# Optimization experiments

Measured on AMD Instinct MI355X. Metric: run time of the kernel, lower is better.

Reference implementation:

```python
import jax, jax.numpy as jnp
import numpy as np

ALPHA = 5.0  # spatial bandwidth
BETA = 5.0   # feature (bilateral) bandwidth
EPS = 1e-20


def gauss_filter(features, values):
    """Exact dense Gaussian (bilateral) filter: the math the permutohedral
    lattice (pl.apply) approximates.
    features: [B, D, N], values: [B, C, N] -> [B, C, N]
    Q[b,c,i] = sum_j exp(-0.5*||f_i - f_j||^2) * v[b,c,j]
    """
    sq = jnp.sum(features * features, axis=1)  # [B, N]
    d2 = sq[:, :, None] + sq[:, None, :] - 2.0 * jnp.einsum('bdi,bdj->bij', features, features)
    K = jnp.exp(-0.5 * jnp.maximum(d2, 0.0))  # [B, N, N]
    return jnp.einsum('bij,bcj->bci', K, values)


def setup_inputs() -> dict:
    key = jax.random.key(0)
    k1, k2 = jax.random.split(key)
    I = jax.random.normal(k1, (2, 3, 18, 18, 18), dtype=jnp.float32)
    U = jax.random.normal(k2, (2, 4, 18, 18, 18), dtype=jnp.float32)
    return {"I": I, "U": U}


def reference(I, U):
    B, n_feat, X, Y, Z = I.shape
    N = X * Y * Z
    n_ch = U.shape[1]
    # spatial coordinates, scaled by alpha (smoothness kernel part)
    gx, gy, gz = jnp.meshgrid(jnp.arange(X), jnp.arange(Y), jnp.arange(Z), indexing='ij')
    coords = jnp.stack([gx, gy, gz], 0).astype(I.dtype)            # [3, X, Y, Z]
    coords = jnp.broadcast_to(coords[None], (B, 3, X, Y, Z))
    feats = jnp.concatenate([coords / ALPHA, I / BETA], axis=1)    # [B, 3+n_feat, X, Y, Z]
    feats = feats.reshape(B, n_feat + 3, N)
    # normalization: filter an all-ones signal (use_norm=True path)
    ones = jnp.ones((B, 1, N), dtype=I.dtype)
    spatial_norm = 1.0 / jnp.sqrt(gauss_filter(feats, ones) + EPS)  # [B, 1, N]
    # unary -> softmax over channels
    Uf = U.reshape(B, n_ch, N)
    H1 = jax.nn.softmax(Uf, axis=1)                                 # [B, C, N]
    # pairwise message passing (normalized bilateral filter)
    Q1 = gauss_filter(feats, H1 * spatial_norm) * spatial_norm      # [B, C, N]
    # trace(Q1_flat.T @ (1 - H1_flat)) == elementwise sum (same reshape on both)
    loss = jnp.sum(Q1 * (1.0 - H1))
    return loss
```

## Files before the change

kernel.cpp:

```cpp
#include <hip/hip_runtime.h>

#define B_      2
#define NCH     4
#define DIMX    18
#define NPT     (18*18*18)
#define TIL     183
#define ITIL    184
#define NPTP    (ITIL*32)
#define IBLOCKS 23
#define JSP     22
#define NB      (IBLOCKS*JSP*B_)
#define MAXT    9
#define FSC     (1.2011224087864498f / 5.0f)
#define QPAD    -30000.0f

typedef __attribute__((ext_vector_type(8)))  short short8;
typedef __attribute__((ext_vector_type(16))) float f32x16;
typedef __attribute__((ext_vector_type(4)))  int   int4_;

#define EXP2(x) __builtin_amdgcn_exp2f(x)
#define MFMA32(a, b, c) __builtin_amdgcn_mfma_f32_32x32x16_bf16(a, b, c, 0, 0, 0)

__device__ __forceinline__ unsigned short bf16rtn(float f) {
  unsigned u = __float_as_uint(f);
  u += 0x7fffu + ((u >> 16) & 1u);
  return (unsigned short)(u >> 16);
}
__device__ __forceinline__ float bf2f(unsigned short s) {
  return __uint_as_float(((unsigned)s) << 16);
}

__device__ __forceinline__ float blockReduceSum(float v) {
  #pragma unroll
  for (int o = 32; o > 0; o >>= 1) v += __shfl_down(v, o, 64);
  __shared__ float red[4];
  int wid = threadIdx.x >> 6, lane = threadIdx.x & 63;
  if (lane == 0) red[wid] = v;
  __syncthreads();
  v = (threadIdx.x < 4) ? red[threadIdx.x] : 0.0f;
  if (wid == 0) {
    v += __shfl_down(v, 2, 64);
    v += __shfl_down(v, 1, 64);
  }
  __syncthreads();
  return v;
}

__device__ __forceinline__ void feat6(const float* __restrict__ I, int bb, int n,
                                      float f[6], float* q) {
  int x = n / (DIMX * DIMX);
  int rem = n - x * DIMX * DIMX;
  int y = rem / DIMX, zz = rem - y * DIMX;
  f[0] = x * FSC; f[1] = y * FSC; f[2] = zz * FSC;
  f[3] = I[(size_t)(bb * 3 + 0) * NPT + n] * FSC;
  f[4] = I[(size_t)(bb * 3 + 1) * NPT + n] * FSC;
  f[5] = I[(size_t)(bb * 3 + 2) * NPT + n] * FSC;
  *q = -0.5f * (f[0]*f[0] + f[1]*f[1] + f[2]*f[2] + f[3]*f[3] + f[4]*f[4] + f[5]*f[5]);
}

__device__ __forceinline__ void bfeat(const float* __restrict__ I, int bb, int n,
                                      short8* hi, short8* lo) {
  short8 h_ = {0,0,0,0,0,0,0,0}, l_ = {0,0,0,0,0,0,0,0};
  if (n < NPT) {
    float f[6], q;
    feat6(I, bb, n, f, &q);
    float bv[8] = {f[0], f[1], f[2], f[3], f[4], f[5], 1.0f, q};
    #pragma unroll
    for (int e = 0; e < 8; ++e) {
      unsigned short bh = bf16rtn(bv[e]);
      h_[e] = (short)bh;
      l_[e] = (short)bf16rtn(bv[e] - bf2f(bh));
    }
  } else {
    h_[7] = (short)bf16rtn(QPAD);
  }
  *hi = h_; *lo = l_;
}

__device__ __forceinline__ short8 afeat(const float* __restrict__ I, int bb, int n) {
  short8 a = {0,0,0,0,0,0,0,0};
  if (n < NPT) {
    float f[6], q;
    feat6(I, bb, n, f, &q);
    float av[8] = {f[0], f[1], f[2], f[3], f[4], f[5], q, 1.0f};
    #pragma unroll
    for (int e = 0; e < 8; ++e) a[e] = (short)bf16rtn(av[e]);
  }
  return a;
}

__device__ __forceinline__ float4 softmax4(const float* __restrict__ U, int bb, int n) {
  float u0 = U[(size_t)(bb * NCH + 0) * NPT + n];
  float u1 = U[(size_t)(bb * NCH + 1) * NPT + n];
  float u2 = U[(size_t)(bb * NCH + 2) * NPT + n];
  float u3 = U[(size_t)(bb * NCH + 3) * NPT + n];
  float m = fmaxf(fmaxf(u0, u1), fmaxf(u2, u3));
  float e0 = __expf(u0-m), e1 = __expf(u1-m), e2 = __expf(u2-m), e3 = __expf(u3-m);
  float inv = 1.0f / (e0 + e1 + e2 + e3);
  return make_float4(e0*inv, e1*inv, e2*inv, e3*inv);
}

__device__ __forceinline__ float expsum16(const f32x16 acc) {
  float e[16];
  #pragma unroll
  for (int r = 0; r < 16; ++r) e[r] = EXP2(acc[r]);
  float s8[8];
  #pragma unroll
  for (int r = 0; r < 8; ++r) s8[r] = e[2*r] + e[2*r+1];
  float s4[4];
  #pragma unroll
  for (int r = 0; r < 4; ++r) s4[r] = s8[2*r] + s8[2*r+1];
  return (s4[0] + s4[1]) + (s4[2] + s4[3]);
}

__global__ void __launch_bounds__(256, 4) pass1_kernel(const float* __restrict__ I,
                                                       float* __restrict__ part) {
  __shared__ short8 bhl[MAXT * 32 * 2];
  int tid = threadIdx.x, wid = tid >> 6, l = tid & 63, h = l >> 5, li = l & 31;
  int bb = blockIdx.z, jc = blockIdx.y, ib = blockIdx.x;
  int t0 = jc * TIL / JSP, t1 = (jc + 1) * TIL / JSP;
  int cnt = (t1 - t0) * 32;

  for (int p = tid; p < cnt; p += 256) {
    short8 hi, lo;
    bfeat(I, bb, t0 * 32 + p, &hi, &lo);
    bhl[p * 2]     = hi;
    bhl[p * 2 + 1] = lo;
  }

  int i0 = (ib * 8 + wid) * 32 + li;
  int i1 = i0 + 128;
  short8 b1_0 = afeat(I, bb, i0);
  short8 b1_1 = afeat(I, bb, i1);
  __syncthreads();

  f32x16 z;
  #pragma unroll
  for (int r = 0; r < 16; ++r) z[r] = 0.0f;

  float sacc0 = 0.0f, sacc1 = 0.0f;
  for (int t = t0; t < t1; ++t) {
    short8 a = bhl[((t - t0) * 32 + li) * 2 + h];
    f32x16 acc0 = MFMA32(a, b1_0, z);
    f32x16 acc1 = MFMA32(a, b1_1, z);
    sacc0 += expsum16(acc0);
    sacc1 += expsum16(acc1);
  }
  sacc0 += __shfl_xor(sacc0, 32, 64);
  sacc1 += __shfl_xor(sacc1, 32, 64);
  if (h == 0) {
    part[((size_t)bb * JSP + jc) * NPTP + i0] = sacc0;
    part[((size_t)bb * JSP + jc) * NPTP + i1] = sacc1;
  }
}

__global__ void __launch_bounds__(256, 4) pass2_kernel(const float* __restrict__ I,
                                                       const float* __restrict__ U,
                                                       const float* __restrict__ part,
                                                       float* __restrict__ pl,
                                                       unsigned* __restrict__ cnt_,
                                                       float* __restrict__ out) {
  __shared__ short8 bhl[MAXT * 32 * 2];
  __shared__ short8 vt8[MAXT * 4 * 4];
  __shared__ bool isLast;
  int tid = threadIdx.x, wid = tid >> 6, l = tid & 63, h = l >> 5, li = l & 31;
  int bb = blockIdx.z, jc = blockIdx.y, ib = blockIdx.x;
  int t0 = jc * TIL / JSP, t1 = (jc + 1) * TIL / JSP;
  int cnt = (t1 - t0) * 32;
  unsigned short* vtp = (unsigned short*)vt8;

  for (int p = tid; p < cnt; p += 256) {
    int j = t0 * 32 + p;
    short8 hi, lo;
    bfeat(I, bb, j, &hi, &lo);
    bhl[p * 2]     = hi;
    bhl[p * 2 + 1] = lo;
    float4 hv = make_float4(0.f, 0.f, 0.f, 0.f);
    float nrm = 0.0f;
    if (j < NPT) {
      float s = 0.0f;
      #pragma unroll
      for (int k = 0; k < JSP; ++k) s += part[((size_t)bb * JSP + k) * NPTP + j];
      nrm = rsqrtf(s + 1e-20f);
      hv = softmax4(U, bb, j);
    }
    int tt = p >> 5, jj = p & 31;
    int g1 = jj >> 4, r = jj & 15;
    int slot = (g1 * 2 + ((r >> 2) & 1)) * 8 + (r & 3) + 4 * (r >> 3);
    vtp[(tt * 4 + 0) * 32 + slot] = bf16rtn(hv.x * nrm);
    vtp[(tt * 4 + 1) * 32 + slot] = bf16rtn(hv.y * nrm);
    vtp[(tt * 4 + 2) * 32 + slot] = bf16rtn(hv.z * nrm);
    vtp[(tt * 4 + 3) * 32 + slot] = bf16rtn(hv.w * nrm);
  }

  int i0 = (ib * 8 + wid) * 32 + li;
  int i1 = i0 + 128;
  short8 b1_0 = afeat(I, bb, i0);
  short8 b1_1 = afeat(I, bb, i1);
  float4 g0 = make_float4(0.f, 0.f, 0.f, 0.f), g1v = g0;
  {
    if (i0 < NPT) {
      float s = 0.0f;
      #pragma unroll
      for (int k = 0; k < JSP; ++k) s += part[((size_t)bb * JSP + k) * NPTP + i0];
      float nrm = rsqrtf(s + 1e-20f);
      float4 hh = softmax4(U, bb, i0);
      g0 = make_float4((1.f-hh.x)*nrm, (1.f-hh.y)*nrm, (1.f-hh.z)*nrm, (1.f-hh.w)*nrm);
    }
    if (i1 < NPT) {
      float s = 0.0f;
      #pragma unroll
      for (int k = 0; k < JSP; ++k) s += part[((size_t)bb * JSP + k) * NPTP + i1];
      float nrm = rsqrtf(s + 1e-20f);
      float4 hh = softmax4(U, bb, i1);
      g1v = make_float4((1.f-hh.x)*nrm, (1.f-hh.y)*nrm, (1.f-hh.z)*nrm, (1.f-hh.w)*nrm);
    }
  }
  __syncthreads();

  const short8 zer = {0, 0, 0, 0, 0, 0, 0, 0};
  bool cok = li < 4;
  int cc = cok ? li : 0;

  f32x16 z;
  #pragma unroll
  for (int r = 0; r < 16; ++r) z[r] = 0.0f;
  f32x16 d2_0 = z, d2_1 = z;

  for (int t = t0; t < t1; ++t) {
    int tt = t - t0;
    short8 a = bhl[(tt * 32 + li) * 2 + h];
    short8 vf1 = vt8[(tt * 4 + cc) * 4 + h];
    short8 vf2 = vt8[(tt * 4 + cc) * 4 + 2 + h];
    vf1 = cok ? vf1 : zer;
    vf2 = cok ? vf2 : zer;

    f32x16 acc0 = MFMA32(a, b1_0, z);
    f32x16 acc1 = MFMA32(a, b1_1, z);

    float w0[16], w1[16];
    #pragma unroll
    for (int r = 0; r < 16; ++r) { w0[r] = EXP2(acc0[r]); w1[r] = EXP2(acc1[r]); }
    int p0[8], p1[8];
    #pragma unroll
    for (int r = 0; r < 8; ++r) {
      asm("v_cvt_pk_bf16_f32 %0, %1, %2" : "=v"(p0[r]) : "v"(w0[2*r]), "v"(w0[2*r+1]));
      asm("v_cvt_pk_bf16_f32 %0, %1, %2" : "=v"(p1[r]) : "v"(w1[2*r]), "v"(w1[2*r+1]));
    }
    union { int4_ iv; short8 sv; } u1a, u2a, u1b, u2b;
    u1a.iv = (int4_){p0[0], p0[1], p0[2], p0[3]};
    u2a.iv = (int4_){p0[4], p0[5], p0[6], p0[7]};
    u1b.iv = (int4_){p1[0], p1[1], p1[2], p1[3]};
    u2b.iv = (int4_){p1[4], p1[5], p1[6], p1[7]};

    d2_0 = MFMA32(vf1, u1a.sv, d2_0);
    d2_0 = MFMA32(vf2, u2a.sv, d2_0);
    d2_1 = MFMA32(vf1, u1b.sv, d2_1);
    d2_1 = MFMA32(vf2, u2b.sv, d2_1);
  }

  float loss = d2_0[0] * g0.x + d2_0[1] * g0.y + d2_0[2] * g0.z + d2_0[3] * g0.w
             + d2_1[0] * g1v.x + d2_1[1] * g1v.y + d2_1[2] * g1v.z + d2_1[3] * g1v.w;
  float r = blockReduceSum(loss);

  int blkflat = ((bb * JSP + jc) * IBLOCKS + ib);
  if (tid == 0) {
    pl[blkflat] = r;
    __threadfence();
    unsigned prev = atomicAdd(cnt_, 1u);
    isLast = (prev == NB - 1);
  }
  __syncthreads();
  if (isLast) {
    __threadfence();
    float v = 0.0f;
    for (int k = tid; k < NB; k += 256) v += pl[k];
    float rr = blockReduceSum(v);
    if (tid == 0) out[0] = rr;
  }
}

extern "C" void kernel_launch(void* const* d_in, const int* in_sizes, int n_in,
                              void* d_out, int out_size, void* d_ws, size_t ws_size,
                              hipStream_t stream) {
  const float* I = (const float*)d_in[0];
  const float* U = (const float*)d_in[1];
  float* out = (float*)d_out;

  char* w = (char*)d_ws;
  float* part = (float*)w;          w += (size_t)B_ * JSP * NPTP * 4;
  float* pl   = (float*)w;          w += (size_t)NB * 4;
  unsigned* cnt_ = (unsigned*)w;    w += 64;

  hipMemsetAsync(cnt_, 0, 4, stream);
  dim3 grid(IBLOCKS, JSP, B_);
  pass1_kernel<<<grid, 256, 0, stream>>>(I, part);
  pass2_kernel<<<grid, 256, 0, stream>>>(I, U, part, pl, cnt_, out);
}
```

Measured before the change: 48.34 us.

## Fuse normalization and message passes into one kernel with a grid-wide barrier

Merges the two kernel launches into one persistent kernel. An atomic counter spin-barrier separates the normalization-sum phase from the filtering phase, and the shared-memory feature tile is reused across both. The j-split is halved so the grid (506 blocks) can be co-resident, which a software grid barrier needs to avoid deadlock. In exchange each block does more serial work, parallelism drops, and the barrier adds spin latency.

```diff
diff --git a/kernel.cpp b/kernel.cpp
--- a/kernel.cpp
+++ b/kernel.cpp
@@ -8,9 +8,9 @@
 #define ITIL    184
 #define NPTP    (ITIL*32)
 #define IBLOCKS 23
-#define JSP     22
+#define JSP     11
 #define NB      (IBLOCKS*JSP*B_)
-#define MAXT    9
+#define MAXT    17
 #define FSC     (1.2011224087864498f / 5.0f)
 #define QPAD    -30000.0f
 
@@ -20,6 +20,13 @@
 
 #define EXP2(x) __builtin_amdgcn_exp2f(x)
 #define MFMA32(a, b, c) __builtin_amdgcn_mfma_f32_32x32x16_bf16(a, b, c, 0, 0, 0)
+
+__device__ __forceinline__ void g_store(float* p, float v) {
+  __hip_atomic_store(p, v, __ATOMIC_RELAXED, __HIP_MEMORY_SCOPE_AGENT);
+}
+__device__ __forceinline__ float g_load(const float* p) {
+  return __hip_atomic_load(p, __ATOMIC_RELAXED, __HIP_MEMORY_SCOPE_AGENT);
+}
 
 __device__ __forceinline__ unsigned short bf16rtn(float f) {
   unsigned u = __float_as_uint(f);
@@ -113,74 +120,74 @@
   return (s4[0] + s4[1]) + (s4[2] + s4[3]);
 }
 
-__global__ void __launch_bounds__(256, 4) pass1_kernel(const float* __restrict__ I,
-                                                       float* __restrict__ part) {
-  __shared__ short8 bhl[MAXT * 32 * 2];
-  int tid = threadIdx.x, wid = tid >> 6, l = tid & 63, h = l >> 5, li = l & 31;
-  int bb = blockIdx.z, jc = blockIdx.y, ib = blockIdx.x;
-  int t0 = jc * TIL / JSP, t1 = (jc + 1) * TIL / JSP;
-  int cnt = (t1 - t0) * 32;
-
-  for (int p = tid; p < cnt; p += 256) {
-    short8 hi, lo;
-    bfeat(I, bb, t0 * 32 + p, &hi, &lo);
-    bhl[p * 2]     = hi;
-    bhl[p * 2 + 1] = lo;
-  }
-
-  int i0 = (ib * 8 + wid) * 32 + li;
-  int i1 = i0 + 128;
-  short8 b1_0 = afeat(I, bb, i0);
-  short8 b1_1 = afeat(I, bb, i1);
-  __syncthreads();
-
-  f32x16 z;
-  #pragma unroll
-  for (int r = 0; r < 16; ++r) z[r] = 0.0f;
-
-  float sacc0 = 0.0f, sacc1 = 0.0f;
-  for (int t = t0; t < t1; ++t) {
-    short8 a = bhl[((t - t0) * 32 + li) * 2 + h];
-    f32x16 acc0 = MFMA32(a, b1_0, z);
-    f32x16 acc1 = MFMA32(a, b1_1, z);
-    sacc0 += expsum16(acc0);
-    sacc1 += expsum16(acc1);
-  }
-  sacc0 += __shfl_xor(sacc0, 32, 64);
-  sacc1 += __shfl_xor(sacc1, 32, 64);
-  if (h == 0) {
-    part[((size_t)bb * JSP + jc) * NPTP + i0] = sacc0;
-    part[((size_t)bb * JSP + jc) * NPTP + i1] = sacc1;
-  }
-}
-
-__global__ void __launch_bounds__(256, 4) pass2_kernel(const float* __restrict__ I,
-                                                       const float* __restrict__ U,
-                                                       const float* __restrict__ part,
-                                                       float* __restrict__ pl,
-                                                       unsigned* __restrict__ cnt_,
-                                                       float* __restrict__ out) {
+__global__ void init_kernel(unsigned* __restrict__ cnt_) {
+  if (threadIdx.x < 2) cnt_[threadIdx.x] = 0;
+}
+
+__global__ void __launch_bounds__(256, 2)
+fused_kernel(const float* __restrict__ I, const float* __restrict__ U,
+             float* __restrict__ part, float* __restrict__ pl,
+             unsigned* __restrict__ cnt_, float* __restrict__ out) {
   __shared__ short8 bhl[MAXT * 32 * 2];
   __shared__ short8 vt8[MAXT * 4 * 4];
   __shared__ bool isLast;
   int tid = threadIdx.x, wid = tid >> 6, l = tid & 63, h = l >> 5, li = l & 31;
   int bb = blockIdx.z, jc = blockIdx.y, ib = blockIdx.x;
   int t0 = jc * TIL / JSP, t1 = (jc + 1) * TIL / JSP;
-  int cnt = (t1 - t0) * 32;
+  int npts = (t1 - t0) * 32;
   unsigned short* vtp = (unsigned short*)vt8;
 
-  for (int p = tid; p < cnt; p += 256) {
-    int j = t0 * 32 + p;
+  for (int p = tid; p < npts; p += 256) {
     short8 hi, lo;
-    bfeat(I, bb, j, &hi, &lo);
+    bfeat(I, bb, t0 * 32 + p, &hi, &lo);
     bhl[p * 2]     = hi;
     bhl[p * 2 + 1] = lo;
+  }
+  int i0 = (ib * 8 + wid) * 32 + li;
+  int i1 = i0 + 128;
+  short8 b1_0 = afeat(I, bb, i0);
+  short8 b1_1 = afeat(I, bb, i1);
+  __syncthreads();
+
+  f32x16 z;
+  #pragma unroll
+  for (int r = 0; r < 16; ++r) z[r] = 0.0f;
+
+  {
+    float sacc0 = 0.0f, sacc1 = 0.0f;
+    for (int t = t0; t < t1; ++t) {
+      short8 a = bhl[((t - t0) * 32 + li) * 2 + h];
+      f32x16 acc0 = MFMA32(a, b1_0, z);
+      f32x16 acc1 = MFMA32(a, b1_1, z);
+      sacc0 += expsum16(acc0);
+      sacc1 += expsum16(acc1);
+    }
+    sacc0 += __shfl_xor(sacc0, 32, 64);
+    sacc1 += __shfl_xor(sacc1, 32, 64);
+    if (h == 0) {
+      g_store(&part[((size_t)bb * JSP + jc) * NPTP + i0], sacc0);
+      g_store(&part[((size_t)bb * JSP + jc) * NPTP + i1], sacc1);
+    }
+  }
+
+  __syncthreads();
+  if (tid == 0) {
+    __threadfence();
+    __hip_atomic_fetch_add(&cnt_[0], 1u, __ATOMIC_ACQ_REL, __HIP_MEMORY_SCOPE_AGENT);
+    while (__hip_atomic_load(&cnt_[0], __ATOMIC_ACQUIRE, __HIP_MEMORY_SCOPE_AGENT) < NB)
+      __builtin_amdgcn_s_sleep(2);
+  }
+  __syncthreads();
+  __threadfence();
+
+  for (int p = tid; p < npts; p += 256) {
+    int j = t0 * 32 + p;
     float4 hv = make_float4(0.f, 0.f, 0.f, 0.f);
     float nrm = 0.0f;
     if (j < NPT) {
       float s = 0.0f;
       #pragma unroll
-      for (int k = 0; k < JSP; ++k) s += part[((size_t)bb * JSP + k) * NPTP + j];
+      for (int k = 0; k < JSP; ++k) s += g_load(&part[((size_t)bb * JSP + k) * NPTP + j]);
       nrm = rsqrtf(s + 1e-20f);
       hv = softmax4(U, bb, j);
     }
@@ -192,39 +199,28 @@
     vtp[(tt * 4 + 2) * 32 + slot] = bf16rtn(hv.z * nrm);
     vtp[(tt * 4 + 3) * 32 + slot] = bf16rtn(hv.w * nrm);
   }
-
-  int i0 = (ib * 8 + wid) * 32 + li;
-  int i1 = i0 + 128;
-  short8 b1_0 = afeat(I, bb, i0);
-  short8 b1_1 = afeat(I, bb, i1);
   float4 g0 = make_float4(0.f, 0.f, 0.f, 0.f), g1v = g0;
-  {
-    if (i0 < NPT) {
-      float s = 0.0f;
-      #pragma unroll
-      for (int k = 0; k < JSP; ++k) s += part[((size_t)bb * JSP + k) * NPTP + i0];
-      float nrm = rsqrtf(s + 1e-20f);
-      float4 hh = softmax4(U, bb, i0);
-      g0 = make_float4((1.f-hh.x)*nrm, (1.f-hh.y)*nrm, (1.f-hh.z)*nrm, (1.f-hh.w)*nrm);
-    }
-    if (i1 < NPT) {
-      float s = 0.0f;
-      #pragma unroll
-      for (int k = 0; k < JSP; ++k) s += part[((size_t)bb * JSP + k) * NPTP + i1];
-      float nrm = rsqrtf(s + 1e-20f);
-      float4 hh = softmax4(U, bb, i1);
-      g1v = make_float4((1.f-hh.x)*nrm, (1.f-hh.y)*nrm, (1.f-hh.z)*nrm, (1.f-hh.w)*nrm);
-    }
+  if (i0 < NPT) {
+    float s = 0.0f;
+    #pragma unroll
+    for (int k = 0; k < JSP; ++k) s += g_load(&part[((size_t)bb * JSP + k) * NPTP + i0]);
+    float nrm = rsqrtf(s + 1e-20f);
+    float4 hh = softmax4(U, bb, i0);
+    g0 = make_float4((1.f-hh.x)*nrm, (1.f-hh.y)*nrm, (1.f-hh.z)*nrm, (1.f-hh.w)*nrm);
+  }
+  if (i1 < NPT) {
+    float s = 0.0f;
+    #pragma unroll
+    for (int k = 0; k < JSP; ++k) s += g_load(&part[((size_t)bb * JSP + k) * NPTP + i1]);
+    float nrm = rsqrtf(s + 1e-20f);
+    float4 hh = softmax4(U, bb, i1);
+    g1v = make_float4((1.f-hh.x)*nrm, (1.f-hh.y)*nrm, (1.f-hh.z)*nrm, (1.f-hh.w)*nrm);
   }
   __syncthreads();
 
   const short8 zer = {0, 0, 0, 0, 0, 0, 0, 0};
   bool cok = li < 4;
   int cc = cok ? li : 0;
-
-  f32x16 z;
-  #pragma unroll
-  for (int r = 0; r < 16; ++r) z[r] = 0.0f;
   f32x16 d2_0 = z, d2_1 = z;
 
   for (int t = t0; t < t1; ++t) {
@@ -265,16 +261,17 @@
 
   int blkflat = ((bb * JSP + jc) * IBLOCKS + ib);
   if (tid == 0) {
-    pl[blkflat] = r;
+    g_store(&pl[blkflat], r);
     __threadfence();
-    unsigned prev = atomicAdd(cnt_, 1u);
+    unsigned prev = __hip_atomic_fetch_add(&cnt_[1], 1u, __ATOMIC_ACQ_REL,
+                                           __HIP_MEMORY_SCOPE_AGENT);
     isLast = (prev == NB - 1);
   }
   __syncthreads();
   if (isLast) {
     __threadfence();
     float v = 0.0f;
-    for (int k = tid; k < NB; k += 256) v += pl[k];
+    for (int k = tid; k < NB; k += 256) v += g_load(&pl[k]);
     float rr = blockReduceSum(v);
     if (tid == 0) out[0] = rr;
   }
@@ -292,8 +289,7 @@
   float* pl   = (float*)w;          w += (size_t)NB * 4;
   unsigned* cnt_ = (unsigned*)w;    w += 64;
 
-  hipMemsetAsync(cnt_, 0, 4, stream);
+  init_kernel<<<1, 64, 0, stream>>>(cnt_);
   dim3 grid(IBLOCKS, JSP, B_);
-  pass1_kernel<<<grid, 256, 0, stream>>>(I, part);
-  pass2_kernel<<<grid, 256, 0, stream>>>(I, U, part, pl, cnt_, out);
-}
+  fused_kernel<<<grid, 256, 0, stream>>>(I, U, part, pl, cnt_, out);
+}
```

After: 96.80 us. +100.2%, slower.

## Precompute normalized softmax values in separate finalize kernel; widen j-chunks

Applied to the files above, without the earlier changes.

Adds a finalize kernel that reduces the partial normalization sums once per point and writes the bf16 normalized softmax values and the (1-H)*norm weights to global buffers. Before, every pass2 block recomputed the JSP-way reduction and the softmax for its j-tile and its i-rows. pass2 now streams V from global memory through an ldv helper instead of staging it in shared memory. The j-split is also cut from 22 to 16 chunks, which lowers the grid size and the reduction depth, and the occupancy hint in launch_bounds is removed. The cost is one extra kernel launch plus global-memory traffic for the intermediate buffers.

```diff
diff --git a/kernel.cpp b/kernel.cpp
--- a/kernel.cpp
+++ b/kernel.cpp
@@ -8,13 +8,14 @@
 #define ITIL    184
 #define NPTP    (ITIL*32)
 #define IBLOCKS 23
-#define JSP     22
+#define JSP     16
 #define NB      (IBLOCKS*JSP*B_)
-#define MAXT    9
+#define MAXT    12
 #define FSC     (1.2011224087864498f / 5.0f)
 #define QPAD    -30000.0f
 
 typedef __attribute__((ext_vector_type(8)))  short short8;
+typedef __attribute__((ext_vector_type(4)))  short short4_;
 typedef __attribute__((ext_vector_type(16))) float f32x16;
 typedef __attribute__((ext_vector_type(4)))  int   int4_;
 
@@ -113,21 +114,20 @@
   return (s4[0] + s4[1]) + (s4[2] + s4[3]);
 }
 
-__global__ void __launch_bounds__(256, 4) pass1_kernel(const float* __restrict__ I,
-                                                       float* __restrict__ part) {
+__global__ void __launch_bounds__(256) pass1_kernel(const float* __restrict__ I,
+                                                    float* __restrict__ part) {
   __shared__ short8 bhl[MAXT * 32 * 2];
   int tid = threadIdx.x, wid = tid >> 6, l = tid & 63, h = l >> 5, li = l & 31;
   int bb = blockIdx.z, jc = blockIdx.y, ib = blockIdx.x;
   int t0 = jc * TIL / JSP, t1 = (jc + 1) * TIL / JSP;
-  int cnt = (t1 - t0) * 32;
-
-  for (int p = tid; p < cnt; p += 256) {
+  int npts = (t1 - t0) * 32;
+
+  for (int p = tid; p < npts; p += 256) {
     short8 hi, lo;
     bfeat(I, bb, t0 * 32 + p, &hi, &lo);
     bhl[p * 2]     = hi;
     bhl[p * 2 + 1] = lo;
   }
-
   int i0 = (ib * 8 + wid) * 32 + li;
   int i1 = i0 + 128;
   short8 b1_0 = afeat(I, bb, i0);
@@ -154,73 +154,77 @@
   }
 }
 
-__global__ void __launch_bounds__(256, 4) pass2_kernel(const float* __restrict__ I,
-                                                       const float* __restrict__ U,
-                                                       const float* __restrict__ part,
-                                                       float* __restrict__ pl,
-                                                       unsigned* __restrict__ cnt_,
-                                                       float* __restrict__ out) {
+__global__ void finalize_kernel(const float* __restrict__ U, const float* __restrict__ part,
+                                unsigned short* __restrict__ Vt, float4* __restrict__ G4) {
+  int idx = blockIdx.x * 256 + threadIdx.x;
+  if (idx >= B_ * NPTP) return;
+  int bb = idx / NPTP, ii = idx - bb * NPTP;
+  if (ii < NPT) {
+    float s = 0.0f;
+    #pragma unroll
+    for (int k = 0; k < JSP; ++k) s += part[((size_t)bb * JSP + k) * NPTP + ii];
+    float nrm = rsqrtf(s + 1e-20f);
+    float4 hh = softmax4(U, bb, ii);
+    Vt[((size_t)bb * 4 + 0) * NPTP + ii] = bf16rtn(hh.x * nrm);
+    Vt[((size_t)bb * 4 + 1) * NPTP + ii] = bf16rtn(hh.y * nrm);
+    Vt[((size_t)bb * 4 + 2) * NPTP + ii] = bf16rtn(hh.z * nrm);
+    Vt[((size_t)bb * 4 + 3) * NPTP + ii] = bf16rtn(hh.w * nrm);
+    G4[idx] = make_float4((1.0f - hh.x) * nrm, (1.0f - hh.y) * nrm,
+                          (1.0f - hh.z) * nrm, (1.0f - hh.w) * nrm);
+  } else {
+    Vt[((size_t)bb * 4 + 0) * NPTP + ii] = 0;
+    Vt[((size_t)bb * 4 + 1) * NPTP + ii] = 0;
+    Vt[((size_t)bb * 4 + 2) * NPTP + ii] = 0;
+    Vt[((size_t)bb * 4 + 3) * NPTP + ii] = 0;
+    G4[idx] = make_float4(0.f, 0.f, 0.f, 0.f);
+  }
+}
+
+__device__ __forceinline__ void ldv(const unsigned short* __restrict__ vrow, int j32,
+                                    int h, bool cok, short8* vf1, short8* vf2) {
+  const short4_ zer4 = {0, 0, 0, 0};
+  short4_ va = cok ? *(const short4_*)(vrow + j32 + 4*h)      : zer4;
+  short4_ vb = cok ? *(const short4_*)(vrow + j32 + 8 + 4*h)  : zer4;
+  short4_ vc = cok ? *(const short4_*)(vrow + j32 + 16 + 4*h) : zer4;
+  short4_ vd = cok ? *(const short4_*)(vrow + j32 + 24 + 4*h) : zer4;
+  short8 f1, f2;
+  #pragma unroll
+  for (int e = 0; e < 4; ++e) {
+    f1[e] = va[e]; f1[4 + e] = vb[e];
+    f2[e] = vc[e]; f2[4 + e] = vd[e];
+  }
+  *vf1 = f1; *vf2 = f2;
+}
+
+__global__ void __launch_bounds__(256) pass2_kernel(const float* __restrict__ I,
+                                                    const unsigned short* __restrict__ Vt,
+                                                    const float4* __restrict__ G4,
+                                                    float* __restrict__ pl,
+                                                    unsigned* __restrict__ cnt_,
+                                                    float* __restrict__ out) {
   __shared__ short8 bhl[MAXT * 32 * 2];
-  __shared__ short8 vt8[MAXT * 4 * 4];
   __shared__ bool isLast;
   int tid = threadIdx.x, wid = tid >> 6, l = tid & 63, h = l >> 5, li = l & 31;
   int bb = blockIdx.z, jc = blockIdx.y, ib = blockIdx.x;
   int t0 = jc * TIL / JSP, t1 = (jc + 1) * TIL / JSP;
-  int cnt = (t1 - t0) * 32;
-  unsigned short* vtp = (unsigned short*)vt8;
-
-  for (int p = tid; p < cnt; p += 256) {
-    int j = t0 * 32 + p;
+  int npts = (t1 - t0) * 32;
+
+  for (int p = tid; p < npts; p += 256) {
     short8 hi, lo;
-    bfeat(I, bb, j, &hi, &lo);
+    bfeat(I, bb, t0 * 32 + p, &hi, &lo);
     bhl[p * 2]     = hi;
     bhl[p * 2 + 1] = lo;
-    float4 hv = make_float4(0.f, 0.f, 0.f, 0.f);
-    float nrm = 0.0f;
-    if (j < NPT) {
-      float s = 0.0f;
-      #pragma unroll
-      for (int k = 0; k < JSP; ++k) s += part[((size_t)bb * JSP + k) * NPTP + j];
-      nrm = rsqrtf(s + 1e-20f);
-      hv = softmax4(U, bb, j);
-    }
-    int tt = p >> 5, jj = p & 31;
-    int g1 = jj >> 4, r = jj & 15;
-    int slot = (g1 * 2 + ((r >> 2) & 1)) * 8 + (r & 3) + 4 * (r >> 3);
-    vtp[(tt * 4 + 0) * 32 + slot] = bf16rtn(hv.x * nrm);
-    vtp[(tt * 4 + 1) * 32 + slot] = bf16rtn(hv.y * nrm);
-    vtp[(tt * 4 + 2) * 32 + slot] = bf16rtn(hv.z * nrm);
-    vtp[(tt * 4 + 3) * 32 + slot] = bf16rtn(hv.w * nrm);
-  }
-
+  }
   int i0 = (ib * 8 + wid) * 32 + li;
   int i1 = i0 + 128;
   short8 b1_0 = afeat(I, bb, i0);
   short8 b1_1 = afeat(I, bb, i1);
-  float4 g0 = make_float4(0.f, 0.f, 0.f, 0.f), g1v = g0;
-  {
-    if (i0 < NPT) {
-      float s = 0.0f;
-      #pragma unroll
-      for (int k = 0; k < JSP; ++k) s += part[((size_t)bb * JSP + k) * NPTP + i0];
-      float nrm = rsqrtf(s + 1e-20f);
-      float4 hh = softmax4(U, bb, i0);
-      g0 = make_float4((1.f-hh.x)*nrm, (1.f-hh.y)*nrm, (1.f-hh.z)*nrm, (1.f-hh.w)*nrm);
-    }
-    if (i1 < NPT) {
-      float s = 0.0f;
-      #pragma unroll
-      for (int k = 0; k < JSP; ++k) s += part[((size_t)bb * JSP + k) * NPTP + i1];
-      float nrm = rsqrtf(s + 1e-20f);
-      float4 hh = softmax4(U, bb, i1);
-      g1v = make_float4((1.f-hh.x)*nrm, (1.f-hh.y)*nrm, (1.f-hh.z)*nrm, (1.f-hh.w)*nrm);
-    }
-  }
-  __syncthreads();
-
-  const short8 zer = {0, 0, 0, 0, 0, 0, 0, 0};
+  size_t pbase = (size_t)bb * NPTP;
+  float4 g0 = G4[pbase + i0];
+  float4 g1v = G4[pbase + i1];
   bool cok = li < 4;
-  int cc = cok ? li : 0;
+  const unsigned short* vrow = Vt + ((size_t)bb * 4 + (cok ? li : 0)) * NPTP;
+  __syncthreads();
 
   f32x16 z;
   #pragma unroll
@@ -228,12 +232,9 @@
   f32x16 d2_0 = z, d2_1 = z;
 
   for (int t = t0; t < t1; ++t) {
-    int tt = t - t0;
-    short8 a = bhl[(tt * 32 + li) * 2 + h];
-    short8 vf1 = vt8[(tt * 4 + cc) * 4 + h];
-    short8 vf2 = vt8[(tt * 4 + cc) * 4 + 2 + h];
-    vf1 = cok ? vf1 : zer;
-    vf2 = cok ? vf2 : zer;
+    short8 a = bhl[((t - t0) * 32 + li) * 2 + h];
+    short8 vf1, vf2;
+    ldv(vrow, t * 32, h, cok, &vf1, &vf2);
 
     f32x16 acc0 = MFMA32(a, b1_0, z);
     f32x16 acc1 = MFMA32(a, b1_1, z);
@@ -288,12 +289,15 @@
   float* out = (float*)d_out;
 
   char* w = (char*)d_ws;
-  float* part = (float*)w;          w += (size_t)B_ * JSP * NPTP * 4;
-  float* pl   = (float*)w;          w += (size_t)NB * 4;
-  unsigned* cnt_ = (unsigned*)w;    w += 64;
+  float* part = (float*)w;                  w += (size_t)B_ * JSP * NPTP * 4;
+  unsigned short* Vt = (unsigned short*)w;  w += (size_t)B_ * 4 * NPTP * 2;
+  float4* G4  = (float4*)w;                 w += (size_t)B_ * NPTP * 16;
+  float*  pl  = (float*)w;                  w += (size_t)NB * 4;
+  unsigned* cnt_ = (unsigned*)w;            w += 64;
 
   hipMemsetAsync(cnt_, 0, 4, stream);
   dim3 grid(IBLOCKS, JSP, B_);
   pass1_kernel<<<grid, 256, 0, stream>>>(I, part);
-  pass2_kernel<<<grid, 256, 0, stream>>>(I, U, part, pl, cnt_, out);
-}
+  finalize_kernel<<<(B_ * NPTP + 255) / 256, 256, 0, stream>>>(U, part, Vt, G4);
+  pass2_kernel<<<grid, 256, 0, stream>>>(I, Vt, G4, pl, cnt_, out);
+}
```

After: 49.93 us. +3.3%, slower.
